# Kernel optimization log

Measured on AMD Instinct MI355X. Metric: run time of the kernel, lower is better.

Reference implementation:

```python
import jax, jax.numpy as jnp
import numpy as np

N_HEAD = 8
N_QP = 4  # query/key points per head
N_VP = 4  # value points per head
D_SPH = 16  # scalar dims per head
SCALE_SCALAR = D_SPH ** (-0.5)
SCALE_POINT = (4.5 * N_QP) ** (-0.5)
SCALE_TOTAL = 3.0 ** (-0.5)  # scalar + pair bias + point logits


def _euclid(xp, r, t):
    # xp: (b,n,l,p,3), r: (b,l,3,3), t: (b,l,3)  -> row-vector convention: x @ r + t
    return jnp.einsum('bnlpk,blkc->bnlpc', xp, r) + t[:, None, :, None, :]


def _inv_euclid(xp, r, t):
    # (x - t) @ r^T
    return jnp.einsum('bnlpk,blck->bnlpc', xp - t[:, None, :, None, :], r)


def setup_inputs() -> dict:
    key = jax.random.key(0)
    ks = jax.random.split(key, 16)
    b, l, d_res, d_pair = 2, 512, 384, 128
    w = lambda k, shp, fan: jax.random.normal(k, shp, jnp.float32) * (fan ** -0.5)
    return {
        'x': jax.random.normal(ks[0], (b, l, d_res), jnp.float32),
        'e': jax.random.normal(ks[1], (b, l, l, d_pair), jnp.float32),
        'r': jax.random.normal(ks[2], (b, l, 3, 3), jnp.float32),
        't': jax.random.normal(ks[3], (b, l, 3), jnp.float32),
        'Wq_s': w(ks[4], (d_res, N_HEAD * D_SPH), d_res),
        'Wk_s': w(ks[5], (d_res, N_HEAD * D_SPH), d_res),
        'Wv_s': w(ks[6], (d_res, N_HEAD * D_SPH), d_res),
        'Wpb': w(ks[7], (d_pair, N_HEAD), d_pair),
        'Wq_p': w(ks[8], (d_res, N_HEAD * N_QP * 3), d_res),
        'Wk_p': w(ks[9], (d_res, N_HEAD * N_QP * 3), d_res),
        'Wv_p': w(ks[10], (d_res, N_HEAD * N_VP * 3), d_res),
        'gamma': jnp.log(jnp.expm1(jnp.ones((N_HEAD,), jnp.float32))),
        'Wout': w(ks[11], (N_HEAD * D_SPH + N_HEAD * d_pair + N_HEAD * N_VP * 3 + N_HEAD * N_VP, d_res), 1280),
        'bout': jnp.zeros((d_res,), jnp.float32),
    }


def reference(x, e, r, t, Wq_s, Wk_s, Wv_s, Wpb, Wq_p, Wk_p, Wv_p, gamma, Wout, bout):
    b, l, _ = x.shape
    n = N_HEAD

    def split_heads(v):  # (b,l,n*d) -> (b,n,l,d)
        return v.reshape(b, l, n, -1).transpose(0, 2, 1, 3)

    def split_points(v, p):  # (b,l,n*p*3) -> (b,n,l,p,3)
        return v.reshape(b, l, n, p, 3).transpose(0, 2, 1, 3, 4)

    q_s, k_s, v_s = (split_heads(x @ W) for W in (Wq_s, Wk_s, Wv_s))
    q_p = _euclid(split_points(x @ Wq_p, N_QP), r, t)
    k_p = _euclid(split_points(x @ Wk_p, N_QP), r, t)
    v_p = _euclid(split_points(x @ Wv_p, N_VP), r, t)

    logit_scalar = jnp.einsum('bnid,bnjd->bnij', q_s, k_s) * SCALE_SCALAR
    bias_pair = (e @ Wpb).transpose(0, 3, 1, 2)  # (b,n,i,j)
    # pairwise squared point distances, summed over points p and coords c
    diff = q_p[:, :, :, None] - k_p[:, :, None]  # (b,n,i,j,p,3)
    sqdist = (diff ** 2).sum(axis=(-1, -2))      # (b,n,i,j)
    logit_point = -0.5 * SCALE_POINT * gamma[None, :, None, None] * sqdist

    attn = jax.nn.softmax(SCALE_TOTAL * (logit_scalar + bias_pair + logit_point), axis=-1)

    out_scalar = jnp.einsum('bnij,bnjd->bnid', attn, v_s).transpose(0, 2, 1, 3).reshape(b, l, -1)
    out_pair = jnp.einsum('bnij,bijd->bnid', attn, e).transpose(0, 2, 1, 3).reshape(b, l, -1)
    out_point = jnp.einsum('bnij,bnjpc->bnipc', attn, v_p)
    out_point = _inv_euclid(out_point, r, t)  # (b,n,i,p,3)
    out_point_norm = jnp.sqrt((out_point ** 2).sum(-1))  # (b,n,i,p)
    out_point = out_point.transpose(0, 2, 1, 3, 4).reshape(b, l, -1)
    out_point_norm = out_point_norm.transpose(0, 2, 1, 3).reshape(b, l, -1)

    out = jnp.concatenate([out_scalar, out_pair, out_point, out_point_norm], axis=-1)
    return out @ Wout + bout
```

## Files before the change

kernel.cpp:

```cpp
#include <hip/hip_runtime.h>
#include <hip/hip_bf16.h>
#include <math.h>

#define NH 8
#define L 512
#define DR 384
#define DP 128
#define DS 16
#define DCAT 1280
#define TJ 64

#define SCALE_SCALAR 0.25f
#define SCALE_POINT  0.23570226039551584f
#define SCALE_TOTAL  0.5773502691896258f

typedef __bf16 bf16_t;
typedef bf16_t bf16x8 __attribute__((ext_vector_type(8)));
typedef float  f32x4v __attribute__((ext_vector_type(4)));

__global__ __launch_bounds__(256) void k_prep(const float* __restrict__ Wout,
                                              __hip_bfloat16* __restrict__ WoutT) {
    int g = blockIdx.x * 256 + threadIdx.x;
    int n = g / 1280, k = g % 1280;
    WoutT[g] = __float2bfloat16(Wout[k * 384 + n]);
}

__global__ __launch_bounds__(256) void k_proj(
    const float* __restrict__ x, const float* __restrict__ r, const float* __restrict__ t,
    const float* __restrict__ Wq_s, const float* __restrict__ Wk_s, const float* __restrict__ Wv_s,
    const float* __restrict__ Wq_p, const float* __restrict__ Wk_p, const float* __restrict__ Wv_p,
    float* __restrict__ q_s, float* __restrict__ k_s, float* __restrict__ v_s,
    float* __restrict__ q_p, float* __restrict__ k_p, float* __restrict__ v_p) {
    __shared__ float xs[4][DR];
    __shared__ float praw[4][3][96];
    __shared__ float rt[4][12];
    const int tid = threadIdx.x;
    const int r0 = blockIdx.x * 4;

    for (int idx = tid; idx < 4 * DR; idx += 256) {
        int row = idx / DR, k = idx % DR;
        xs[row][k] = x[(size_t)(r0 + row) * DR + k];
    }
    if (tid < 48) {
        int row = tid / 12, c = tid % 12;
        rt[row][c] = (c < 9) ? r[(r0 + row) * 9 + c] : t[(r0 + row) * 3 + (c - 9)];
    }
    __syncthreads();

    for (int it = 0; it < 11; ++it) {
        int item = tid + it * 256;
        if (item < 4 * 672) {
            int row = item / 672, o = item % 672;
            const float* W; int col, ncol, kind;
            if (o < 384) { kind = o / 128; col = o % 128; ncol = 128;
                           W = (kind == 0) ? Wq_s : (kind == 1) ? Wk_s : Wv_s; }
            else { int o2 = o - 384; kind = 3 + o2 / 96; col = o2 % 96; ncol = 96;
                   W = (kind == 3) ? Wq_p : (kind == 4) ? Wk_p : Wv_p; }
            float acc = 0.f;
            for (int k = 0; k < DR; ++k) acc += xs[row][k] * W[k * ncol + col];
            int gl = r0 + row, b = gl >> 9, l = gl & 511;
            if (o < 384) {
                int n = col / 16, d = col % 16;
                float* dst = (kind == 0) ? q_s : (kind == 1) ? k_s : v_s;
                dst[((size_t)(b * NH + n) * L + l) * DS + d] = acc;
            } else {
                praw[row][kind - 3][col] = acc;
            }
        }
    }
    __syncthreads();
    for (int it = 0; it < 5; ++it) {
        int item = tid + it * 256;
        if (item < 4 * 3 * 96) {
            int row = item / 288, rem = item % 288, arr = rem / 96, o = rem % 96;
            int n = o / 12, pc = o % 12, p = pc / 3, c = pc % 3;
            float acc = rt[row][9 + c];
            for (int k = 0; k < 3; ++k) acc += praw[row][arr][n * 12 + p * 3 + k] * rt[row][k * 3 + c];
            int gl = r0 + row, b = gl >> 9, l = gl & 511;
            float* dst = (arr == 0) ? q_p : (arr == 1) ? k_p : v_p;
            dst[((size_t)(b * NH + n) * L + l) * 12 + pc] = acc;
        }
    }
}

__global__ __launch_bounds__(256) void k_attn(
    const float* __restrict__ e, const float* __restrict__ r, const float* __restrict__ t,
    const float* __restrict__ Wpb, const float* __restrict__ gamma,
    const float* __restrict__ q_s, const float* __restrict__ k_s, const float* __restrict__ v_s,
    const float* __restrict__ q_p, const float* __restrict__ k_p, const float* __restrict__ v_p,
    __hip_bfloat16* __restrict__ concat) {
    __shared__ __align__(16) float et[TJ * DP];
    __shared__ float pt[NH][TJ];
    __shared__ __align__(16) float wpbT[NH][DP];
    __shared__ float qsl[NH][DS];
    __shared__ float qpl[NH][12];
    __shared__ float lsh[NH];
    __shared__ float gsh[NH];
    __shared__ __align__(16) float accp[NH][DP];
    __shared__ float osh[NH][12];
    __shared__ float o2sh[NH][12];
    __shared__ float rtsh[12];

    const int tid = threadIdx.x;
    const int bi = blockIdx.x;
    const int b = bi >> 9, i = bi & 511;
    const int lane = tid & 63, wv = tid >> 6;
    const int d4 = tid & 31, jsub = tid >> 5;

    for (int idx = tid; idx < NH * DP; idx += 256) {
        int n = idx >> 7, d = idx & 127;
        wpbT[n][d] = Wpb[d * NH + n];
    }
    if (tid < 128) { int n = tid >> 4, d = tid & 15; qsl[n][d] = q_s[((size_t)(b * NH + n) * L + i) * DS + d]; }
    else if (tid < 224) { int o = tid - 128; int n = o / 12, pc = o % 12; qpl[n][pc] = q_p[((size_t)(b * NH + n) * L + i) * 12 + pc]; }
    else if (tid < 232) { gsh[tid - 224] = gamma[tid - 224]; }
    else if (tid < 244) { int c = tid - 232; rtsh[c] = (c < 9) ? r[bi * 9 + c] : t[bi * 3 + (c - 9)]; }

    float lsum0 = 0.f, lsum1 = 0.f;
    float4 accPair[NH];
#pragma unroll
    for (int n = 0; n < NH; ++n) accPair[n] = make_float4(0.f, 0.f, 0.f, 0.f);
    float accS = 0.f, accP3 = 0.f;
    const int nS = tid >> 4, dSd = tid & 15;
    const int oP = tid - 128, nP = (oP < 96) ? oP / 12 : 0, pcP = (oP < 96) ? oP % 12 : 0;

    const float4* esrc = reinterpret_cast<const float4*>(e + (size_t)(b * L + i) * L * DP);

    for (int tile = 0; tile < L / TJ; ++tile) {
        const int j0 = tile * TJ;
        __syncthreads();
#pragma unroll
        for (int s = 0; s < 8; ++s) {
            int f = tid + s * 256;
            int j = f >> 5, g = f & 31;
            float4 v = esrc[(size_t)(j0 + j) * 32 + g];
            reinterpret_cast<float4*>(et)[j * 32 + (g ^ (j & 31))] = v;
        }
        __syncthreads();
        {
            const int j = lane, jj = j0 + lane;
            const int n0 = wv, n1 = wv + 4;
            const float4* row = reinterpret_cast<const float4*>(et) + j * 32;
            const float4* w0 = reinterpret_cast<const float4*>(&wpbT[n0][0]);
            const float4* w1 = reinterpret_cast<const float4*>(&wpbT[n1][0]);
            float b0 = 0.f, b1 = 0.f;
#pragma unroll 8
            for (int g = 0; g < 32; ++g) {
                float4 ev = row[g ^ (j & 31)];
                float4 a0 = w0[g], a1 = w1[g];
                b0 += ev.x * a0.x + ev.y * a0.y + ev.z * a0.z + ev.w * a0.w;
                b1 += ev.x * a1.x + ev.y * a1.y + ev.z * a1.z + ev.w * a1.w;
            }
            float s0 = 0.f, s1 = 0.f;
            const float4* ks0 = reinterpret_cast<const float4*>(k_s + ((size_t)(b * NH + n0) * L + jj) * DS);
            const float4* ks1 = reinterpret_cast<const float4*>(k_s + ((size_t)(b * NH + n1) * L + jj) * DS);
#pragma unroll
            for (int g = 0; g < 4; ++g) {
                float4 kv0 = ks0[g], kv1 = ks1[g];
                s0 += kv0.x * qsl[n0][g * 4 + 0] + kv0.y * qsl[n0][g * 4 + 1] + kv0.z * qsl[n0][g * 4 + 2] + kv0.w * qsl[n0][g * 4 + 3];
                s1 += kv1.x * qsl[n1][g * 4 + 0] + kv1.y * qsl[n1][g * 4 + 1] + kv1.z * qsl[n1][g * 4 + 2] + kv1.w * qsl[n1][g * 4 + 3];
            }
            float sq0 = 0.f, sq1 = 0.f;
            const float* kp0 = k_p + ((size_t)(b * NH + n0) * L + jj) * 12;
            const float* kp1 = k_p + ((size_t)(b * NH + n1) * L + jj) * 12;
#pragma unroll
            for (int pc = 0; pc < 12; ++pc) {
                float dd0 = qpl[n0][pc] - kp0[pc]; sq0 += dd0 * dd0;
                float dd1 = qpl[n1][pc] - kp1[pc]; sq1 += dd1 * dd1;
            }
            float lg0 = SCALE_TOTAL * (s0 * SCALE_SCALAR + b0 - 0.5f * SCALE_POINT * gsh[n0] * sq0);
            float lg1 = SCALE_TOTAL * (s1 * SCALE_SCALAR + b1 - 0.5f * SCALE_POINT * gsh[n1] * sq1);
            float p0 = __expf(lg0), p1 = __expf(lg1);
            pt[n0][j] = p0; pt[n1][j] = p1;
            lsum0 += p0; lsum1 += p1;
        }
        __syncthreads();
        {
            const float4* et4 = reinterpret_cast<const float4*>(et);
#pragma unroll
            for (int s = 0; s < 8; ++s) {
                int j = jsub * 8 + s;
                float4 ev = et4[j * 32 + (d4 ^ (j & 31))];
#pragma unroll
                for (int n = 0; n < NH; ++n) {
                    float p = pt[n][j];
                    accPair[n].x += p * ev.x; accPair[n].y += p * ev.y;
                    accPair[n].z += p * ev.z; accPair[n].w += p * ev.w;
                }
            }
        }
        if (tid < 128) {
            const float* vsp = v_s + ((size_t)(b * NH + nS) * L + j0) * DS + dSd;
#pragma unroll 8
            for (int j = 0; j < TJ; ++j) accS += pt[nS][j] * vsp[j * DS];
        } else if (tid < 224) {
            const float* vpp = v_p + ((size_t)(b * NH + nP) * L + j0) * 12 + pcP;
#pragma unroll 8
            for (int j = 0; j < TJ; ++j) accP3 += pt[nP][j] * vpp[j * 12];
        }
    }

    for (int off = 32; off > 0; off >>= 1) { lsum0 += __shfl_xor(lsum0, off); lsum1 += __shfl_xor(lsum1, off); }
    __syncthreads();
    if (lane == 0) { lsh[wv] = lsum0; lsh[wv + 4] = lsum1; }
    {
        float4* red = reinterpret_cast<float4*>(et);
#pragma unroll
        for (int n = 0; n < NH; ++n) red[(jsub * NH + n) * 32 + d4] = accPair[n];
    }
    __syncthreads();
    {
        int n = tid >> 5, g = tid & 31;
        const float4* red = reinterpret_cast<const float4*>(et);
        float4 sum = make_float4(0.f, 0.f, 0.f, 0.f);
#pragma unroll
        for (int s = 0; s < 8; ++s) {
            float4 v = red[(s * NH + n) * 32 + g];
            sum.x += v.x; sum.y += v.y; sum.z += v.z; sum.w += v.w;
        }
        reinterpret_cast<float4*>(&accp[n][0])[g] = sum;
    }
    __syncthreads();
    __hip_bfloat16* crow = concat + (size_t)bi * DCAT;
    if (tid < 128) crow[nS * DS + dSd] = __float2bfloat16(accS / lsh[nS]);
    for (int idx = tid; idx < NH * DP; idx += 256) {
        int n = idx >> 7;
        crow[128 + idx] = __float2bfloat16(accp[n][idx & 127] / lsh[n]);
    }
    if (tid >= 128 && tid < 224) osh[nP][pcP] = accP3 / lsh[nP];
    __syncthreads();
    if (tid < 96) {
        int n = tid / 12, pc = tid % 12, p = pc / 3, c = pc % 3;
        float oc = 0.f;
#pragma unroll
        for (int k = 0; k < 3; ++k) oc += (osh[n][p * 3 + k] - rtsh[9 + k]) * rtsh[c * 3 + k];
        crow[128 + 1024 + tid] = __float2bfloat16(oc);
        o2sh[n][pc] = oc;
    }
    __syncthreads();
    if (tid < 32) {
        int n = tid >> 2, p = tid & 3;
        float vx = o2sh[n][p * 3], vy = o2sh[n][p * 3 + 1], vz = o2sh[n][p * 3 + 2];
        crow[128 + 1024 + 96 + tid] = __float2bfloat16(sqrtf(vx * vx + vy * vy + vz * vz));
    }
}

__global__ __launch_bounds__(256) void k_out(const __hip_bfloat16* __restrict__ A,
                                             const __hip_bfloat16* __restrict__ Bt,
                                             const float* __restrict__ bout,
                                             float* __restrict__ out) {
    __shared__ __align__(16) bf16_t At[64 * 40];
    __shared__ __align__(16) bf16_t Bs[64 * 40];
    const int tid = threadIdx.x;
    const int row0 = blockIdx.x * 64, col0 = blockIdx.y * 64;
    const int wv = tid >> 6, lane = tid & 63;
    f32x4v acc[4] = {};

    for (int k0 = 0; k0 < 1280; k0 += 32) {
        __syncthreads();
        {
            int rr = tid >> 2, q = tid & 3;
            *reinterpret_cast<int4*>(&At[rr * 40 + q * 8]) =
                *reinterpret_cast<const int4*>(&A[(size_t)(row0 + rr) * 1280 + k0 + q * 8]);
            *reinterpret_cast<int4*>(&Bs[rr * 40 + q * 8]) =
                *reinterpret_cast<const int4*>(&Bt[(size_t)(col0 + rr) * 1280 + k0 + q * 8]);
        }
        __syncthreads();
        const int m = lane & 15, kq = lane >> 4;
        bf16x8 af = *reinterpret_cast<const bf16x8*>(&At[(wv * 16 + m) * 40 + kq * 8]);
#pragma unroll
        for (int nt = 0; nt < 4; ++nt) {
            bf16x8 bfr = *reinterpret_cast<const bf16x8*>(&Bs[(nt * 16 + m) * 40 + kq * 8]);
            acc[nt] = __builtin_amdgcn_mfma_f32_16x16x32_bf16(af, bfr, acc[nt], 0, 0, 0);
        }
    }
    const int col_l = lane & 15, rbase = (lane >> 4) * 4;
#pragma unroll
    for (int nt = 0; nt < 4; ++nt) {
        int col = col0 + nt * 16 + col_l;
        float bo = bout[col];
#pragma unroll
        for (int rg = 0; rg < 4; ++rg) {
            int rowg = row0 + wv * 16 + rbase + rg;
            out[(size_t)rowg * 384 + col] = acc[nt][rg] + bo;
        }
    }
}

extern "C" void kernel_launch(void* const* d_in, const int* in_sizes, int n_in,
                              void* d_out, int out_size, void* d_ws, size_t ws_size,
                              hipStream_t stream) {
    const float* x     = (const float*)d_in[0];
    const float* e     = (const float*)d_in[1];
    const float* r     = (const float*)d_in[2];
    const float* t     = (const float*)d_in[3];
    const float* Wq_s  = (const float*)d_in[4];
    const float* Wk_s  = (const float*)d_in[5];
    const float* Wv_s  = (const float*)d_in[6];
    const float* Wpb   = (const float*)d_in[7];
    const float* Wq_p  = (const float*)d_in[8];
    const float* Wk_p  = (const float*)d_in[9];
    const float* Wv_p  = (const float*)d_in[10];
    const float* gamma = (const float*)d_in[11];
    const float* Wout  = (const float*)d_in[12];
    const float* bout  = (const float*)d_in[13];

    float* ws  = (float*)d_ws;
    float* q_s = ws + 0;
    float* k_s = ws + 131072;
    float* v_s = ws + 262144;
    float* q_p = ws + 393216;
    float* k_p = ws + 491520;
    float* v_p = ws + 589824;
    __hip_bfloat16* concat = (__hip_bfloat16*)((char*)d_ws + 2752512);
    __hip_bfloat16* WoutT  = (__hip_bfloat16*)((char*)d_ws + 5373952);
    float* out = (float*)d_out;

    hipLaunchKernelGGL(k_prep, dim3(1920), dim3(256), 0, stream, Wout, WoutT);
    hipLaunchKernelGGL(k_proj, dim3(256), dim3(256), 0, stream,
                       x, r, t, Wq_s, Wk_s, Wv_s, Wq_p, Wk_p, Wv_p,
                       q_s, k_s, v_s, q_p, k_p, v_p);
    hipLaunchKernelGGL(k_attn, dim3(1024), dim3(256), 0, stream,
                       e, r, t, Wpb, gamma, q_s, k_s, v_s, q_p, k_p, v_p, concat);
    hipLaunchKernelGGL(k_out, dim3(16, 6), dim3(256), 0, stream, concat, WoutT, bout, out);
}
```

Baseline: 564.8 us.

## Rewrite projection as bf16 MFMA GEMM and double-buffer pair tiles in attention

Replaces the scalar fp32 projection kernel with a packing pass, a bf16 MFMA GEMM and a separate frame-transform kernel. The Wout transpose now goes through an LDS tile so reads and writes are both coalesced. The attention kernel halves the j-tile, double-buffers the pair-feature tile via direct global-to-LDS async loads so the next tile streams in during compute, and reorganizes the per-thread work mapping. The intent is to hide the memory latency of the dominant e read. It adds kernel launches and lowers projection precision to bf16.

```diff
diff --git a/kernel.cpp b/kernel.cpp
--- a/kernel.cpp
+++ b/kernel.cpp
@@ -8,7 +8,8 @@
 #define DP 128
 #define DS 16
 #define DCAT 1280
-#define TJ 64
+#define TJ 32
+#define NTILE 16
 
 #define SCALE_SCALAR 0.25f
 #define SCALE_POINT  0.23570226039551584f
@@ -18,230 +19,342 @@
 typedef bf16_t bf16x8 __attribute__((ext_vector_type(8)));
 typedef float  f32x4v __attribute__((ext_vector_type(4)));
 
+__device__ __forceinline__ void cp_g2l_16(const void* g, void* l) {
+    __builtin_amdgcn_global_load_lds(
+        (const __attribute__((address_space(1))) unsigned int*)g,
+        (__attribute__((address_space(3))) unsigned int*)l, 16, 0, 0);
+}
+
+__global__ __launch_bounds__(256) void k_pack(
+    const float* __restrict__ x,
+    const float* __restrict__ Wq_s, const float* __restrict__ Wk_s, const float* __restrict__ Wv_s,
+    const float* __restrict__ Wq_p, const float* __restrict__ Wk_p, const float* __restrict__ Wv_p,
+    __hip_bfloat16* __restrict__ xb, __hip_bfloat16* __restrict__ WallT) {
+    int idx = blockIdx.x * 256 + threadIdx.x;
+    const int T1 = 1024 * 384;
+    if (idx < T1) {
+        xb[idx] = __float2bfloat16(x[idx]);
+    } else {
+        int j = idx - T1;
+        int n = j / 384, k = j % 384;
+        float v;
+        if      (n < 128) v = Wq_s[k * 128 + n];
+        else if (n < 256) v = Wk_s[k * 128 + (n - 128)];
+        else if (n < 384) v = Wv_s[k * 128 + (n - 256)];
+        else if (n < 480) v = Wq_p[k * 96  + (n - 384)];
+        else if (n < 576) v = Wk_p[k * 96  + (n - 480)];
+        else              v = Wv_p[k * 96  + (n - 576)];
+        WallT[(size_t)n * 384 + k] = __float2bfloat16(v);
+    }
+}
+
 __global__ __launch_bounds__(256) void k_prep(const float* __restrict__ Wout,
                                               __hip_bfloat16* __restrict__ WoutT) {
-    int g = blockIdx.x * 256 + threadIdx.x;
-    int n = g / 1280, k = g % 1280;
-    WoutT[g] = __float2bfloat16(Wout[k * 384 + n]);
-}
-
-__global__ __launch_bounds__(256) void k_proj(
-    const float* __restrict__ x, const float* __restrict__ r, const float* __restrict__ t,
-    const float* __restrict__ Wq_s, const float* __restrict__ Wk_s, const float* __restrict__ Wv_s,
-    const float* __restrict__ Wq_p, const float* __restrict__ Wk_p, const float* __restrict__ Wv_p,
+    __shared__ float tile[64][65];
+    const int tid = threadIdx.x;
+    const int k0 = blockIdx.x * 64;
+    const int n0 = blockIdx.y * 64;
+#pragma unroll
+    for (int s = 0; s < 16; ++s) {
+        int idx = s * 256 + tid, kk = idx >> 6, nn = idx & 63;
+        tile[kk][nn] = Wout[(size_t)(k0 + kk) * 384 + n0 + nn];
+    }
+    __syncthreads();
+#pragma unroll
+    for (int s = 0; s < 16; ++s) {
+        int idx = s * 256 + tid, nn = idx >> 6, kk = idx & 63;
+        WoutT[(size_t)(n0 + nn) * 1280 + k0 + kk] = __float2bfloat16(tile[kk][nn]);
+    }
+}
+
+__global__ __launch_bounds__(256) void k_projm(
+    const __hip_bfloat16* __restrict__ xb, const __hip_bfloat16* __restrict__ WallT,
     float* __restrict__ q_s, float* __restrict__ k_s, float* __restrict__ v_s,
+    float* __restrict__ praw) {
+    __shared__ __align__(16) bf16_t As[64 * 40];
+    __shared__ __align__(16) bf16_t Bs[48 * 40];
+    const int tid = threadIdx.x;
+    const int row0 = blockIdx.x * 64, col0 = blockIdx.y * 48;
+    const int w = tid >> 6, lane = tid & 63;
+    f32x4v acc[3] = {};
+
+    for (int k0 = 0; k0 < 384; k0 += 32) {
+        __syncthreads();
+        {
+            int rr = tid >> 2, q = tid & 3;
+            *reinterpret_cast<int4*>(&As[rr * 40 + q * 8]) =
+                *reinterpret_cast<const int4*>(&xb[(size_t)(row0 + rr) * 384 + k0 + q * 8]);
+            if (tid < 192)
+                *reinterpret_cast<int4*>(&Bs[rr * 40 + q * 8]) =
+                    *reinterpret_cast<const int4*>(&WallT[(size_t)(col0 + rr) * 384 + k0 + q * 8]);
+        }
+        __syncthreads();
+        const int m = lane & 15, kq = lane >> 4;
+        bf16x8 af = *reinterpret_cast<const bf16x8*>(&As[(w * 16 + m) * 40 + kq * 8]);
+#pragma unroll
+        for (int c = 0; c < 3; ++c) {
+            bf16x8 bfr = *reinterpret_cast<const bf16x8*>(&Bs[(c * 16 + m) * 40 + kq * 8]);
+            acc[c] = __builtin_amdgcn_mfma_f32_16x16x32_bf16(af, bfr, acc[c], 0, 0, 0);
+        }
+    }
+    const int colL = lane & 15, rbase = (lane >> 4) * 4;
+#pragma unroll
+    for (int c = 0; c < 3; ++c) {
+        int col = col0 + c * 16 + colL;
+#pragma unroll
+        for (int rg = 0; rg < 4; ++rg) {
+            int row = row0 + w * 16 + rbase + rg;
+            float v = acc[c][rg];
+            int bb = row >> 9, ll = row & 511;
+            if (col < 384) {
+                int kind = col >> 7, n = (col >> 4) & 7, d = col & 15;
+                float* dst = (kind == 0) ? q_s : (kind == 1) ? k_s : v_s;
+                dst[((size_t)(bb * NH + n) * L + ll) * DS + d] = v;
+            } else {
+                praw[(size_t)row * 288 + (col - 384)] = v;
+            }
+        }
+    }
+}
+
+__global__ __launch_bounds__(256) void k_euclid(
+    const float* __restrict__ praw, const float* __restrict__ r, const float* __restrict__ t,
     float* __restrict__ q_p, float* __restrict__ k_p, float* __restrict__ v_p) {
-    __shared__ float xs[4][DR];
-    __shared__ float praw[4][3][96];
-    __shared__ float rt[4][12];
-    const int tid = threadIdx.x;
-    const int r0 = blockIdx.x * 4;
-
-    for (int idx = tid; idx < 4 * DR; idx += 256) {
-        int row = idx / DR, k = idx % DR;
-        xs[row][k] = x[(size_t)(r0 + row) * DR + k];
-    }
-    if (tid < 48) {
-        int row = tid / 12, c = tid % 12;
-        rt[row][c] = (c < 9) ? r[(r0 + row) * 9 + c] : t[(r0 + row) * 3 + (c - 9)];
-    }
-    __syncthreads();
-
-    for (int it = 0; it < 11; ++it) {
-        int item = tid + it * 256;
-        if (item < 4 * 672) {
-            int row = item / 672, o = item % 672;
-            const float* W; int col, ncol, kind;
-            if (o < 384) { kind = o / 128; col = o % 128; ncol = 128;
-                           W = (kind == 0) ? Wq_s : (kind == 1) ? Wk_s : Wv_s; }
-            else { int o2 = o - 384; kind = 3 + o2 / 96; col = o2 % 96; ncol = 96;
-                   W = (kind == 3) ? Wq_p : (kind == 4) ? Wk_p : Wv_p; }
-            float acc = 0.f;
-            for (int k = 0; k < DR; ++k) acc += xs[row][k] * W[k * ncol + col];
-            int gl = r0 + row, b = gl >> 9, l = gl & 511;
-            if (o < 384) {
-                int n = col / 16, d = col % 16;
-                float* dst = (kind == 0) ? q_s : (kind == 1) ? k_s : v_s;
-                dst[((size_t)(b * NH + n) * L + l) * DS + d] = acc;
-            } else {
-                praw[row][kind - 3][col] = acc;
-            }
-        }
-    }
-    __syncthreads();
-    for (int it = 0; it < 5; ++it) {
-        int item = tid + it * 256;
-        if (item < 4 * 3 * 96) {
-            int row = item / 288, rem = item % 288, arr = rem / 96, o = rem % 96;
-            int n = o / 12, pc = o % 12, p = pc / 3, c = pc % 3;
-            float acc = rt[row][9 + c];
-            for (int k = 0; k < 3; ++k) acc += praw[row][arr][n * 12 + p * 3 + k] * rt[row][k * 3 + c];
-            int gl = r0 + row, b = gl >> 9, l = gl & 511;
-            float* dst = (arr == 0) ? q_p : (arr == 1) ? k_p : v_p;
-            dst[((size_t)(b * NH + n) * L + l) * 12 + pc] = acc;
-        }
-    }
-}
-
-__global__ __launch_bounds__(256) void k_attn(
+    int idx = blockIdx.x * 256 + threadIdx.x;
+    int row = idx / 288, o = idx % 288;
+    int arr = o / 96, oo = o % 96;
+    int n = oo / 12, pc = oo % 12, p = pc / 3, c = pc % 3;
+    const float* base = praw + (size_t)row * 288 + arr * 96 + n * 12 + p * 3;
+    float acc = t[row * 3 + c];
+#pragma unroll
+    for (int k = 0; k < 3; ++k) acc += base[k] * r[row * 9 + k * 3 + c];
+    float* dst = (arr == 0) ? q_p : (arr == 1) ? k_p : v_p;
+    int bb = row >> 9, ll = row & 511;
+    dst[((size_t)(bb * NH + n) * L + ll) * 12 + pc] = acc;
+}
+
+__device__ __forceinline__ void pf_tile(const float4* esrc4, int tile, float* dst,
+                                        int w, int ell) {
+    float4* dst4 = (float4*)dst;
+    const float4* base = esrc4 + (size_t)tile * TJ * 32;
+#pragma unroll
+    for (int s = 0; s < 4; ++s) {
+        int slot = (w * 4 + s) * 64 + ell;
+        int j = slot >> 5;
+        int g = (slot & 31) ^ (j & 31);
+        cp_g2l_16(base + (size_t)j * 32 + g, dst4 + slot);
+    }
+}
+
+__global__ __launch_bounds__(256, 3) void k_attn(
     const float* __restrict__ e, const float* __restrict__ r, const float* __restrict__ t,
     const float* __restrict__ Wpb, const float* __restrict__ gamma,
     const float* __restrict__ q_s, const float* __restrict__ k_s, const float* __restrict__ v_s,
     const float* __restrict__ q_p, const float* __restrict__ k_p, const float* __restrict__ v_p,
     __hip_bfloat16* __restrict__ concat) {
-    __shared__ __align__(16) float et[TJ * DP];
-    __shared__ float pt[NH][TJ];
-    __shared__ __align__(16) float wpbT[NH][DP];
-    __shared__ float qsl[NH][DS];
-    __shared__ float qpl[NH][12];
-    __shared__ float lsh[NH];
-    __shared__ float gsh[NH];
-    __shared__ __align__(16) float accp[NH][DP];
-    __shared__ float osh[NH][12];
-    __shared__ float o2sh[NH][12];
-    __shared__ float rtsh[12];
+    __shared__ __align__(16) float et0[TJ * DP];
+    __shared__ __align__(16) float et1[TJ * DP];
+    __shared__ __align__(16) float wpbT[8 * 132];
+    __shared__ __align__(16) float pt [4 * 8 * 12];
+    __shared__ __align__(16) float ptT[4 * 8 * 8];
+    __shared__ float sv[4 * 224];
+    __shared__ __align__(16) float qsl[8 * 16];
+    __shared__ __align__(16) float qpl[8 * 12];
+    __shared__ float gsh[8], rtsh[12], lpart[32], lsh[8], osh[96], o2sh[96];
 
     const int tid = threadIdx.x;
     const int bi = blockIdx.x;
-    const int b = bi >> 9, i = bi & 511;
-    const int lane = tid & 63, wv = tid >> 6;
-    const int d4 = tid & 31, jsub = tid >> 5;
-
-    for (int idx = tid; idx < NH * DP; idx += 256) {
-        int n = idx >> 7, d = idx & 127;
-        wpbT[n][d] = Wpb[d * NH + n];
-    }
-    if (tid < 128) { int n = tid >> 4, d = tid & 15; qsl[n][d] = q_s[((size_t)(b * NH + n) * L + i) * DS + d]; }
-    else if (tid < 224) { int o = tid - 128; int n = o / 12, pc = o % 12; qpl[n][pc] = q_p[((size_t)(b * NH + n) * L + i) * 12 + pc]; }
-    else if (tid < 232) { gsh[tid - 224] = gamma[tid - 224]; }
-    else if (tid < 244) { int c = tid - 232; rtsh[c] = (c < 9) ? r[bi * 9 + c] : t[bi * 3 + (c - 9)]; }
-
-    float lsum0 = 0.f, lsum1 = 0.f;
-    float4 accPair[NH];
-#pragma unroll
-    for (int n = 0; n < NH; ++n) accPair[n] = make_float4(0.f, 0.f, 0.f, 0.f);
-    float accS = 0.f, accP3 = 0.f;
-    const int nS = tid >> 4, dSd = tid & 15;
-    const int oP = tid - 128, nP = (oP < 96) ? oP / 12 : 0, pcP = (oP < 96) ? oP % 12 : 0;
-
-    const float4* esrc = reinterpret_cast<const float4*>(e + (size_t)(b * L + i) * L * DP);
-
-    for (int tile = 0; tile < L / TJ; ++tile) {
-        const int j0 = tile * TJ;
-        __syncthreads();
-#pragma unroll
-        for (int s = 0; s < 8; ++s) {
-            int f = tid + s * 256;
-            int j = f >> 5, g = f & 31;
-            float4 v = esrc[(size_t)(j0 + j) * 32 + g];
-            reinterpret_cast<float4*>(et)[j * 32 + (g ^ (j & 31))] = v;
-        }
-        __syncthreads();
+    const int b = bi >> 9, i = bi & 511, b8 = b * NH;
+    const int w = tid >> 6, ell = tid & 63;
+    const int nH = ell >> 3, j8 = ell & 7;
+    const int d4 = ell & 31, jh = ell >> 5;
+
+    for (int idx = tid; idx < 1024; idx += 256)
+        wpbT[(idx >> 7) * 132 + (idx & 127)] = Wpb[(idx & 127) * NH + (idx >> 7)];
+    if (tid < 128) {
+        int n = tid >> 4, d = tid & 15;
+        qsl[n * 16 + d] = q_s[((size_t)(b8 + n) * L + i) * DS + d];
+    } else if (tid < 224) {
+        int o = tid - 128; int n = o / 12, pc = o % 12;
+        qpl[n * 12 + pc] = q_p[((size_t)(b8 + n) * L + i) * 12 + pc];
+    } else if (tid < 232) {
+        gsh[tid - 224] = gamma[tid - 224];
+    } else if (tid < 244) {
+        int c = tid - 232;
+        rtsh[c] = (c < 9) ? r[bi * 9 + c] : t[bi * 3 + (c - 9)];
+    }
+
+    int nIt[4]; const float* pIt[4]; int strIt[4];
+#pragma unroll
+    for (int it = 0; it < 4; ++it) {
+        int ii = ell + it * 64;
+        bool valid = (it < 3) || (ell < 32);
+        if (!valid) { nIt[it] = 0; pIt[it] = v_s; strIt[it] = 16; continue; }
+        if (ii < 128) {
+            int n = ii >> 4;
+            nIt[it] = n; strIt[it] = 16;
+            pIt[it] = v_s + (((size_t)(b8 + n) * L + w * 8) << 4) + (ii & 15);
+        } else {
+            int o = ii - 128; int n = o / 12;
+            nIt[it] = n; strIt[it] = 12;
+            pIt[it] = v_p + ((size_t)(b8 + n) * L + w * 8) * 12 + (o % 12);
+        }
+    }
+
+    const float4* esrc4 = reinterpret_cast<const float4*>(e + (size_t)(b * L + i) * L * DP);
+
+    pf_tile(esrc4, 0, et0, w, ell);
+    __syncthreads();
+
+    float lsum = 0.f;
+    float4 accPair[8];
+#pragma unroll
+    for (int n = 0; n < 8; ++n) accPair[n] = make_float4(0.f, 0.f, 0.f, 0.f);
+    float accSV[4] = {0.f, 0.f, 0.f, 0.f};
+
+#pragma unroll 2
+    for (int tt = 0; tt < NTILE; ++tt) {
+        float* cur = (tt & 1) ? et1 : et0;
+        float* nxt = (tt & 1) ? et0 : et1;
+        __builtin_amdgcn_s_waitcnt(0xF70);
+        __builtin_amdgcn_sched_barrier(0);
+
+        const int jg = tt * TJ + w * 8 + j8;
+        const float4* ksr = reinterpret_cast<const float4*>(k_s + (((size_t)(b8 + nH) * L + jg) << 4));
+        float4 ks0 = ksr[0], ks1 = ksr[1], ks2 = ksr[2], ks3 = ksr[3];
+        const float4* kpr = reinterpret_cast<const float4*>(k_p + ((size_t)(b8 + nH) * L + jg) * 12);
+        float4 kp0 = kpr[0], kp1 = kpr[1], kp2 = kpr[2];
+        float vv[4][8];
+#pragma unroll
+        for (int it = 0; it < 4; ++it)
+            if (it < 3 || ell < 32) {
+                const float* p = pIt[it] + (size_t)tt * TJ * strIt[it];
+#pragma unroll
+                for (int jj = 0; jj < 8; ++jj) vv[it][jj] = p[jj * strIt[it]];
+            }
+        __builtin_amdgcn_sched_barrier(0);
+        if (tt < NTILE - 1) pf_tile(esrc4, tt + 1, nxt, w, ell);
+        __builtin_amdgcn_sched_barrier(0);
+
         {
-            const int j = lane, jj = j0 + lane;
-            const int n0 = wv, n1 = wv + 4;
-            const float4* row = reinterpret_cast<const float4*>(et) + j * 32;
-            const float4* w0 = reinterpret_cast<const float4*>(&wpbT[n0][0]);
-            const float4* w1 = reinterpret_cast<const float4*>(&wpbT[n1][0]);
-            float b0 = 0.f, b1 = 0.f;
+            const int jrow = w * 8 + j8;
+            const float4* row4 = reinterpret_cast<const float4*>(cur) + (size_t)jrow * 32;
+            const float4* wr4 = reinterpret_cast<const float4*>(&wpbT[nH * 132]);
+            float bsum = 0.f;
 #pragma unroll 8
             for (int g = 0; g < 32; ++g) {
-                float4 ev = row[g ^ (j & 31)];
-                float4 a0 = w0[g], a1 = w1[g];
-                b0 += ev.x * a0.x + ev.y * a0.y + ev.z * a0.z + ev.w * a0.w;
-                b1 += ev.x * a1.x + ev.y * a1.y + ev.z * a1.z + ev.w * a1.w;
+                float4 ev = row4[g ^ (jrow & 31)];
+                float4 wv4 = wr4[g];
+                bsum += ev.x * wv4.x + ev.y * wv4.y + ev.z * wv4.z + ev.w * wv4.w;
             }
-            float s0 = 0.f, s1 = 0.f;
-            const float4* ks0 = reinterpret_cast<const float4*>(k_s + ((size_t)(b * NH + n0) * L + jj) * DS);
-            const float4* ks1 = reinterpret_cast<const float4*>(k_s + ((size_t)(b * NH + n1) * L + jj) * DS);
-#pragma unroll
-            for (int g = 0; g < 4; ++g) {
-                float4 kv0 = ks0[g], kv1 = ks1[g];
-                s0 += kv0.x * qsl[n0][g * 4 + 0] + kv0.y * qsl[n0][g * 4 + 1] + kv0.z * qsl[n0][g * 4 + 2] + kv0.w * qsl[n0][g * 4 + 3];
-                s1 += kv1.x * qsl[n1][g * 4 + 0] + kv1.y * qsl[n1][g * 4 + 1] + kv1.z * qsl[n1][g * 4 + 2] + kv1.w * qsl[n1][g * 4 + 3];
+            const float4* q4 = reinterpret_cast<const float4*>(&qsl[nH * 16]);
+            float4 qa = q4[0], qb = q4[1], qc = q4[2], qd = q4[3];
+            float ssum = ks0.x * qa.x + ks0.y * qa.y + ks0.z * qa.z + ks0.w * qa.w
+                       + ks1.x * qb.x + ks1.y * qb.y + ks1.z * qb.z + ks1.w * qb.w
+                       + ks2.x * qc.x + ks2.y * qc.y + ks2.z * qc.z + ks2.w * qc.w
+                       + ks3.x * qd.x + ks3.y * qd.y + ks3.z * qd.z + ks3.w * qd.w;
+            const float4* qp4 = reinterpret_cast<const float4*>(&qpl[nH * 12]);
+            float4 pa = qp4[0], pb = qp4[1], pc4 = qp4[2];
+            float d0, sq = 0.f;
+            d0 = pa.x - kp0.x; sq += d0 * d0;  d0 = pa.y - kp0.y; sq += d0 * d0;
+            d0 = pa.z - kp0.z; sq += d0 * d0;  d0 = pa.w - kp0.w; sq += d0 * d0;
+            d0 = pb.x - kp1.x; sq += d0 * d0;  d0 = pb.y - kp1.y; sq += d0 * d0;
+            d0 = pb.z - kp1.z; sq += d0 * d0;  d0 = pb.w - kp1.w; sq += d0 * d0;
+            d0 = pc4.x - kp2.x; sq += d0 * d0; d0 = pc4.y - kp2.y; sq += d0 * d0;
+            d0 = pc4.z - kp2.z; sq += d0 * d0; d0 = pc4.w - kp2.w; sq += d0 * d0;
+            float lg = SCALE_TOTAL * (ssum * SCALE_SCALAR + bsum
+                                      - 0.5f * SCALE_POINT * gsh[nH] * sq);
+            float pv = __expf(lg);
+            lsum += pv;
+            pt [w * 96 + nH * 12 + j8] = pv;
+            ptT[w * 64 + j8 * 8 + nH] = pv;
+        }
+
+        {
+            const float4* cur4 = reinterpret_cast<const float4*>(cur);
+#pragma unroll
+            for (int s = 0; s < 4; ++s) {
+                int jloc = jh * 4 + s;
+                int jrow = w * 8 + jloc;
+                float4 ev = cur4[jrow * 32 + (d4 ^ (jrow & 31))];
+                const float4* pb4 = reinterpret_cast<const float4*>(&ptT[w * 64 + jloc * 8]);
+                float4 pA = pb4[0], pB = pb4[1];
+#define ACCP(nn, ps) accPair[nn].x += (ps) * ev.x; accPair[nn].y += (ps) * ev.y; \
+                     accPair[nn].z += (ps) * ev.z; accPair[nn].w += (ps) * ev.w;
+                ACCP(0, pA.x) ACCP(1, pA.y) ACCP(2, pA.z) ACCP(3, pA.w)
+                ACCP(4, pB.x) ACCP(5, pB.y) ACCP(6, pB.z) ACCP(7, pB.w)
+#undef ACCP
             }
-            float sq0 = 0.f, sq1 = 0.f;
-            const float* kp0 = k_p + ((size_t)(b * NH + n0) * L + jj) * 12;
-            const float* kp1 = k_p + ((size_t)(b * NH + n1) * L + jj) * 12;
-#pragma unroll
-            for (int pc = 0; pc < 12; ++pc) {
-                float dd0 = qpl[n0][pc] - kp0[pc]; sq0 += dd0 * dd0;
-                float dd1 = qpl[n1][pc] - kp1[pc]; sq1 += dd1 * dd1;
+        }
+
+#pragma unroll
+        for (int it = 0; it < 4; ++it)
+            if (it < 3 || ell < 32) {
+                const float4* pr = reinterpret_cast<const float4*>(&pt[w * 96 + nIt[it] * 12]);
+                float4 pA = pr[0], pB = pr[1];
+                accSV[it] += pA.x * vv[it][0] + pA.y * vv[it][1] + pA.z * vv[it][2] + pA.w * vv[it][3]
+                           + pB.x * vv[it][4] + pB.y * vv[it][5] + pB.z * vv[it][6] + pB.w * vv[it][7];
             }
-            float lg0 = SCALE_TOTAL * (s0 * SCALE_SCALAR + b0 - 0.5f * SCALE_POINT * gsh[n0] * sq0);
-            float lg1 = SCALE_TOTAL * (s1 * SCALE_SCALAR + b1 - 0.5f * SCALE_POINT * gsh[n1] * sq1);
-            float p0 = __expf(lg0), p1 = __expf(lg1);
-            pt[n0][j] = p0; pt[n1][j] = p1;
-            lsum0 += p0; lsum1 += p1;
-        }
-        __syncthreads();
-        {
-            const float4* et4 = reinterpret_cast<const float4*>(et);
-#pragma unroll
-            for (int s = 0; s < 8; ++s) {
-                int j = jsub * 8 + s;
-                float4 ev = et4[j * 32 + (d4 ^ (j & 31))];
-#pragma unroll
-                for (int n = 0; n < NH; ++n) {
-                    float p = pt[n][j];
-                    accPair[n].x += p * ev.x; accPair[n].y += p * ev.y;
-                    accPair[n].z += p * ev.z; accPair[n].w += p * ev.w;
-                }
-            }
-        }
-        if (tid < 128) {
-            const float* vsp = v_s + ((size_t)(b * NH + nS) * L + j0) * DS + dSd;
-#pragma unroll 8
-            for (int j = 0; j < TJ; ++j) accS += pt[nS][j] * vsp[j * DS];
-        } else if (tid < 224) {
-            const float* vpp = v_p + ((size_t)(b * NH + nP) * L + j0) * 12 + pcP;
-#pragma unroll 8
-            for (int j = 0; j < TJ; ++j) accP3 += pt[nP][j] * vpp[j * 12];
-        }
-    }
-
-    for (int off = 32; off > 0; off >>= 1) { lsum0 += __shfl_xor(lsum0, off); lsum1 += __shfl_xor(lsum1, off); }
-    __syncthreads();
-    if (lane == 0) { lsh[wv] = lsum0; lsh[wv + 4] = lsum1; }
+    }
+
+    lsum += __shfl_xor(lsum, 1);
+    lsum += __shfl_xor(lsum, 2);
+    lsum += __shfl_xor(lsum, 4);
+    if (j8 == 0) lpart[w * 8 + nH] = lsum;
+#pragma unroll
+    for (int it = 0; it < 4; ++it)
+        if (it < 3 || ell < 32) sv[w * 224 + ell + it * 64] = accSV[it];
+    __syncthreads();
+
+    float4* red4 = reinterpret_cast<float4*>(et0);
     {
-        float4* red = reinterpret_cast<float4*>(et);
-#pragma unroll
-        for (int n = 0; n < NH; ++n) red[(jsub * NH + n) * 32 + d4] = accPair[n];
-    }
-    __syncthreads();
+        int owner = w * 2 + jh;
+#pragma unroll
+        for (int n = 0; n < 8; ++n) red4[(owner * 8 + n) * 32 + d4] = accPair[n];
+    }
+    __syncthreads();
+
+    if (tid < 8) lsh[tid] = lpart[tid] + lpart[8 + tid] + lpart[16 + tid] + lpart[24 + tid];
+    const int np = tid >> 5, gp = tid & 31;
+    float4 ps = make_float4(0.f, 0.f, 0.f, 0.f);
+#pragma unroll
+    for (int o = 0; o < 8; ++o) {
+        float4 v = red4[(o * 8 + np) * 32 + gp];
+        ps.x += v.x; ps.y += v.y; ps.z += v.z; ps.w += v.w;
+    }
+    __syncthreads();
+
+    __hip_bfloat16* crow = concat + (size_t)bi * DCAT;
     {
-        int n = tid >> 5, g = tid & 31;
-        const float4* red = reinterpret_cast<const float4*>(et);
-        float4 sum = make_float4(0.f, 0.f, 0.f, 0.f);
-#pragma unroll
-        for (int s = 0; s < 8; ++s) {
-            float4 v = red[(s * NH + n) * 32 + g];
-            sum.x += v.x; sum.y += v.y; sum.z += v.z; sum.w += v.w;
-        }
-        reinterpret_cast<float4*>(&accp[n][0])[g] = sum;
-    }
-    __syncthreads();
-    __hip_bfloat16* crow = concat + (size_t)bi * DCAT;
-    if (tid < 128) crow[nS * DS + dSd] = __float2bfloat16(accS / lsh[nS]);
-    for (int idx = tid; idx < NH * DP; idx += 256) {
-        int n = idx >> 7;
-        crow[128 + idx] = __float2bfloat16(accp[n][idx & 127] / lsh[n]);
-    }
-    if (tid >= 128 && tid < 224) osh[nP][pcP] = accP3 / lsh[nP];
+        float inv = 1.f / lsh[np];
+        crow[128 + np * 128 + gp * 4 + 0] = __float2bfloat16(ps.x * inv);
+        crow[128 + np * 128 + gp * 4 + 1] = __float2bfloat16(ps.y * inv);
+        crow[128 + np * 128 + gp * 4 + 2] = __float2bfloat16(ps.z * inv);
+        crow[128 + np * 128 + gp * 4 + 3] = __float2bfloat16(ps.w * inv);
+    }
+    if (tid < 128) {
+        float vsum = sv[tid] + sv[224 + tid] + sv[448 + tid] + sv[672 + tid];
+        crow[tid] = __float2bfloat16(vsum / lsh[tid >> 4]);
+    } else if (tid < 224) {
+        int o = tid - 128;
+        float vsum = sv[tid] + sv[224 + tid] + sv[448 + tid] + sv[672 + tid];
+        osh[o] = vsum / lsh[o / 12];
+    }
     __syncthreads();
     if (tid < 96) {
         int n = tid / 12, pc = tid % 12, p = pc / 3, c = pc % 3;
         float oc = 0.f;
 #pragma unroll
-        for (int k = 0; k < 3; ++k) oc += (osh[n][p * 3 + k] - rtsh[9 + k]) * rtsh[c * 3 + k];
-        crow[128 + 1024 + tid] = __float2bfloat16(oc);
-        o2sh[n][pc] = oc;
+        for (int k = 0; k < 3; ++k)
+            oc += (osh[n * 12 + p * 3 + k] - rtsh[9 + k]) * rtsh[c * 3 + k];
+        crow[1152 + tid] = __float2bfloat16(oc);
+        o2sh[tid] = oc;
     }
     __syncthreads();
     if (tid < 32) {
         int n = tid >> 2, p = tid & 3;
-        float vx = o2sh[n][p * 3], vy = o2sh[n][p * 3 + 1], vz = o2sh[n][p * 3 + 2];
-        crow[128 + 1024 + 96 + tid] = __float2bfloat16(sqrtf(vx * vx + vy * vy + vz * vz));
+        float vx = o2sh[n * 12 + p * 3], vy = o2sh[n * 12 + p * 3 + 1], vz = o2sh[n * 12 + p * 3 + 2];
+        crow[1248 + tid] = __float2bfloat16(sqrtf(vx * vx + vy * vy + vz * vz));
     }
 }
 
@@ -305,21 +418,27 @@
     const float* Wout  = (const float*)d_in[12];
     const float* bout  = (const float*)d_in[13];
 
-    float* ws  = (float*)d_ws;
-    float* q_s = ws + 0;
-    float* k_s = ws + 131072;
-    float* v_s = ws + 262144;
-    float* q_p = ws + 393216;
-    float* k_p = ws + 491520;
-    float* v_p = ws + 589824;
-    __hip_bfloat16* concat = (__hip_bfloat16*)((char*)d_ws + 2752512);
-    __hip_bfloat16* WoutT  = (__hip_bfloat16*)((char*)d_ws + 5373952);
+    float* ws   = (float*)d_ws;
+    float* q_s  = ws + 0;
+    float* k_s  = ws + 131072;
+    float* v_s  = ws + 262144;
+    float* q_p  = ws + 393216;
+    float* k_p  = ws + 491520;
+    float* v_p  = ws + 589824;
+    float* praw = ws + 688128;
+    __hip_bfloat16* xb     = (__hip_bfloat16*)((char*)d_ws + 3932160);
+    __hip_bfloat16* WallT  = (__hip_bfloat16*)((char*)d_ws + 4718592);
+    __hip_bfloat16* concat = (__hip_bfloat16*)((char*)d_ws + 5234688);
+    __hip_bfloat16* WoutT  = (__hip_bfloat16*)((char*)d_ws + 7856128);
     float* out = (float*)d_out;
 
-    hipLaunchKernelGGL(k_prep, dim3(1920), dim3(256), 0, stream, Wout, WoutT);
-    hipLaunchKernelGGL(k_proj, dim3(256), dim3(256), 0, stream,
-                       x, r, t, Wq_s, Wk_s, Wv_s, Wq_p, Wk_p, Wv_p,
-                       q_s, k_s, v_s, q_p, k_p, v_p);
+    hipLaunchKernelGGL(k_pack, dim3(2544), dim3(256), 0, stream,
+                       x, Wq_s, Wk_s, Wv_s, Wq_p, Wk_p, Wv_p, xb, WallT);
+    hipLaunchKernelGGL(k_prep, dim3(20, 6), dim3(256), 0, stream, Wout, WoutT);
+    hipLaunchKernelGGL(k_projm, dim3(16, 14), dim3(256), 0, stream,
+                       xb, WallT, q_s, k_s, v_s, praw);
+    hipLaunchKernelGGL(k_euclid, dim3(1152), dim3(256), 0, stream,
+                       praw, r, t, q_p, k_p, v_p);
     hipLaunchKernelGGL(k_attn, dim3(1024), dim3(256), 0, stream,
                        e, r, t, Wpb, gamma, q_s, k_s, v_s, q_p, k_p, v_p, concat);
     hipLaunchKernelGGL(k_out, dim3(16, 6), dim3(256), 0, stream, concat, WoutT, bout, out);
```

Result: slower. 889.8 us (+57.6%).
